# Optimization experiments

Measured on AMD Instinct MI355X. Metric: run time of the kernel, lower is better.

## Reference

```python
import jax, jax.numpy as jnp
import numpy as np

K = 20            # neighbors
C = 21            # num_classes
P = 16            # patch_size
NROWS = 14        # img_size // patch_size
H = NROWS * P     # 224
TEMP = 1.0        # temperature


def setup_inputs() -> dict:
    key = jax.random.key(0)
    k1, k2, k3 = jax.random.split(key, 3)
    test_feature = jax.random.normal(k1, (8, 196, 384), dtype=jnp.float32)
    train_features = jax.random.normal(k2, (384, 50000), dtype=jnp.float32)
    train_labels = jax.random.randint(k3, (256, 50000), 0, C, dtype=jnp.int32)
    return {"test_feature": test_feature, "train_features": train_features,
            "train_labels": train_labels}


def reference(test_feature, train_features, train_labels):
    bs = test_feature.shape[0]
    # similarity: [bs, num_patches, N_train]
    sim = jnp.einsum('bpd,dn->bpn', test_feature, train_features)
    sim_k, idx = jax.lax.top_k(sim, K)              # [bs, 196, K]
    # gather neighbor patch labels: train_labels [P^2, N] -> [bs, 196, K, P^2]
    nb = train_labels.T[idx]
    # make_grid with nrow=NROWS, padding=0: assemble patches into [bs, K, H, H]
    nb = nb.reshape(bs, NROWS, NROWS, K, P, P)
    nb = nb.transpose(0, 3, 1, 4, 2, 5).reshape(bs, K, H, H)
    nb = nb.transpose(0, 2, 3, 1)                   # [bs, H, H, K]
    # weighted majority vote: nearest-upsample similarities 14x14 -> 224x224
    w = sim_k.reshape(bs, NROWS, NROWS, K)
    w = jnp.repeat(jnp.repeat(w, P, axis=1), P, axis=2)   # [bs, H, H, K]
    w = jax.nn.softmax(w / TEMP, axis=-1)
    # one-hot vote expressed as scatter-add over classes (same math, no
    # [bs,H,H,K,C] materialization)
    rows = jnp.arange(bs * H * H)
    vote = jnp.zeros((bs * H * H, C), dtype=w.dtype)
    vote = vote.at[rows[:, None], nb.reshape(bs * H * H, K)].add(
        w.reshape(bs * H * H, K))
    vote = vote.reshape(bs, H, H, C)
    pred = jnp.argmax(vote, axis=-1)                # [bs, H, H] int
    return pred
```

## Files before the change

### kernel.cpp

```cpp
#include <hip/hip_runtime.h>
#include <float.h>

#define N_TRAIN 50000
#define NPAD    50176
#define NBLK    392
#define MPAD    1792
#define DDIM    384
#define M_ROWS  1568
#define KNN     20
#define K2      24
#define SELMAX  64
#define NCLS    21
#define CAPBUF  768
#define CBMAX   256

typedef __attribute__((ext_vector_type(8))) short bf16x8;
typedef __attribute__((ext_vector_type(4))) float f32x4;

static __device__ __forceinline__ unsigned short f2bf(float f) {
  unsigned int u = __float_as_uint(f);
  unsigned int r = (u + 0x7fffu + ((u >> 16) & 1u)) >> 16;
  return (unsigned short)r;
}
static __device__ __forceinline__ unsigned int flip32(unsigned int u) {
  return (u & 0x80000000u) ? ~u : (u | 0x80000000u);
}

__global__ __launch_bounds__(256) void transpose_labels(const int* __restrict__ labels,
                                                        unsigned char* __restrict__ labT) {
  __shared__ int tile[64][65];
  const int t  = threadIdx.x;
  const int c0 = blockIdx.x * 64;
  const int r0 = blockIdx.y * 64;
#pragma unroll
  for (int i = 0; i < 16; ++i) {
    int idx = i * 256 + t;
    int r = idx >> 6, c = idx & 63;
    int cc = c0 + c;
    tile[r][c] = (cc < N_TRAIN) ? labels[(size_t)(r0 + r) * N_TRAIN + cc] : 0;
  }
  __syncthreads();
#pragma unroll
  for (int i = 0; i < 16; ++i) {
    int idx = i * 256 + t;
    int c = idx >> 6, r = idx & 63;
    int cc = c0 + c;
    if (cc < N_TRAIN) labT[(size_t)cc * 256 + r0 + r] = (unsigned char)tile[r][c];
  }
}

__global__ __launch_bounds__(256) void conv_Apack(const float* __restrict__ test,
                                                  unsigned short* __restrict__ Apack) {
  int o = blockIdx.x * 256 + threadIdx.x;
  if (o >= (MPAD / 16) * 12 * 512) return;
  int j = o & 7;
  int l = (o >> 3) & 63;
  int kcmt = o >> 9;
  int kc = kcmt % 12, mt = kcmt / 12;
  int row = mt * 16 + (l & 15);
  int k = kc * 32 + (l >> 4) * 8 + j;
  Apack[o] = (row < M_ROWS) ? f2bf(test[(size_t)row * DDIM + k]) : (unsigned short)0;
}

__global__ __launch_bounds__(256) void trans_train_fused(const float* __restrict__ train,
                                                         unsigned short* __restrict__ Bpack,
                                                         float* __restrict__ trainT) {
  __shared__ float tile[64][65];
  const int t  = threadIdx.x;
  const int c0 = blockIdx.x * 64;
  const int r0 = blockIdx.y * 64;
#pragma unroll
  for (int i = 0; i < 16; ++i) {
    int idx = i * 256 + t;
    int r = idx >> 6, c = idx & 63;
    int cc = c0 + c;
    tile[r][c] = (cc < N_TRAIN) ? train[(size_t)(r0 + r) * N_TRAIN + cc] : 0.f;
  }
  __syncthreads();
#pragma unroll
  for (int it = 0; it < 2; ++it) {
    int u = it * 256 + t;
    int c = u & 63, koctL = u >> 6;
    int col = c0 + c;
    int koct = (r0 >> 3) + koctL;
    int kc = koct >> 2, l4 = koct & 3;
    int nt = col >> 4, l15 = col & 15;
    size_t base = ((size_t)(nt * 12 + kc) * 64 + l4 * 16 + l15) * 8;
    ushort4 h0, h1;
    h0.x = f2bf(tile[koctL * 8 + 0][c]); h0.y = f2bf(tile[koctL * 8 + 1][c]);
    h0.z = f2bf(tile[koctL * 8 + 2][c]); h0.w = f2bf(tile[koctL * 8 + 3][c]);
    h1.x = f2bf(tile[koctL * 8 + 4][c]); h1.y = f2bf(tile[koctL * 8 + 5][c]);
    h1.z = f2bf(tile[koctL * 8 + 6][c]); h1.w = f2bf(tile[koctL * 8 + 7][c]);
    *(ushort4*)&Bpack[base]     = h0;
    *(ushort4*)&Bpack[base + 4] = h1;
  }
#pragma unroll
  for (int i = 0; i < 16; ++i) {
    int idx = i * 256 + t;
    int c = idx >> 6, r = idx & 63;
    int cc = c0 + c;
    if (cc < N_TRAIN) trainT[(size_t)cc * DDIM + r0 + r] = tile[r][c];
  }
}

__global__ __launch_bounds__(256, 2) void mfma_gemm(const unsigned short* __restrict__ Apack,
                                                    const unsigned short* __restrict__ Bpack,
                                                    unsigned short* __restrict__ keybuf,
                                                    unsigned short* __restrict__ blkmax) {
  __shared__ unsigned short ct[128 * 256];
  const int t = threadIdx.x;

  const int flat = blockIdx.x;
  const int wg = (flat & 7) * 343 + (flat >> 3);
  const int mblk = wg % 14, nblk = wg / 14;
  const int m0 = mblk * 128, n0 = nblk * 256;

  const int wc = t >> 6, lane = t & 63;
  const int l15 = lane & 15, l4 = lane >> 4;

  const unsigned short* Ab = Apack + (size_t)(mblk * 8) * 12 * 512;
  const unsigned short* Bb = Bpack + (size_t)(nblk * 16 + wc * 4) * 12 * 512;

  f32x4 acc[8][4];
  const f32x4 zero = {0.f, 0.f, 0.f, 0.f};
#pragma unroll
  for (int f = 0; f < 8; ++f)
#pragma unroll
    for (int n = 0; n < 4; ++n) acc[f][n] = zero;

  for (int kc = 0; kc < 12; ++kc) {
    bf16x8 a[8], b[4];
#pragma unroll
    for (int f = 0; f < 8; ++f)
      a[f] = *(const bf16x8*)&Ab[((size_t)(f * 12 + kc) * 64 + lane) * 8];
#pragma unroll
    for (int n = 0; n < 4; ++n)
      b[n] = *(const bf16x8*)&Bb[((size_t)(n * 12 + kc) * 64 + lane) * 8];
#pragma unroll
    for (int f = 0; f < 8; ++f)
#pragma unroll
      for (int n = 0; n < 4; ++n)
        acc[f][n] = __builtin_amdgcn_mfma_f32_16x16x32_bf16(a[f], b[n], acc[f][n], 0, 0, 0);
  }

#pragma unroll
  for (int f = 0; f < 8; ++f) {
    const int row0 = f * 16 + l4 * 4;
#pragma unroll
    for (int n = 0; n < 4; ++n) {
      const int col = wc * 64 + n * 16 + l15;
      const int cl = col >> 3, ce = col & 7;
#pragma unroll
      for (int r = 0; r < 4; ++r) {
        const int rr = row0 + r;
        unsigned int k16 = flip32(__float_as_uint(acc[f][n][r])) >> 16;
        ct[rr * 256 + ((cl ^ (rr & 31)) << 3) + ce] = (unsigned short)k16;
      }
    }
  }
  __syncthreads();

  const bool boundary = (n0 + 256 > N_TRAIN);
#pragma unroll
  for (int i = 0; i < 16; ++i) {
    int idx = i * 256 + t;
    int row = idx >> 5;
    int cL  = idx & 31;
    uint4 v = *(uint4*)&ct[row * 256 + ((cL ^ (row & 31)) << 3)];
    int c8 = cL * 8;
    if (boundary) {
      int nv = N_TRAIN - (n0 + c8);
      v.x &= ((0 < nv) ? 0x0000FFFFu : 0u) | ((1 < nv) ? 0xFFFF0000u : 0u);
      v.y &= ((2 < nv) ? 0x0000FFFFu : 0u) | ((3 < nv) ? 0xFFFF0000u : 0u);
      v.z &= ((4 < nv) ? 0x0000FFFFu : 0u) | ((5 < nv) ? 0xFFFF0000u : 0u);
      v.w &= ((6 < nv) ? 0x0000FFFFu : 0u) | ((7 < nv) ? 0xFFFF0000u : 0u);
    }
    unsigned int mx = v.x & 0xFFFFu;
    mx = max(mx, v.x >> 16); mx = max(mx, v.y & 0xFFFFu); mx = max(mx, v.y >> 16);
    mx = max(mx, v.z & 0xFFFFu); mx = max(mx, v.z >> 16);
    mx = max(mx, v.w & 0xFFFFu); mx = max(mx, v.w >> 16);
    mx = max(mx, (unsigned int)__shfl_xor((int)mx, 1));
    mx = max(mx, (unsigned int)__shfl_xor((int)mx, 2));
    mx = max(mx, (unsigned int)__shfl_xor((int)mx, 4));
    mx = max(mx, (unsigned int)__shfl_xor((int)mx, 8));
    const int grow = m0 + row;
    if (grow < M_ROWS) {
      if ((lane & 15) == 0) {
        int half = (lane >> 4) & 1;
        blkmax[(size_t)grow * NBLK + nblk * 2 + half] = (unsigned short)mx;
      }
      *(uint4*)&keybuf[(size_t)grow * NPAD + n0 + c8] = v;
    }
  }
}

__global__ __launch_bounds__(256) void tail_fused(const unsigned short* __restrict__ keybuf,
                                                  const unsigned short* __restrict__ blkmax,
                                                  const float* __restrict__ test,
                                                  const float* __restrict__ trainT,
                                                  const unsigned char* __restrict__ labT,
                                                  int* __restrict__ out) {
  const int t = threadIdx.x, m = blockIdx.x;
  __shared__ unsigned short bm[NBLK];
  __shared__ int clist[CBMAX];
  __shared__ int ccnt;
  __shared__ unsigned int smax[256];
  __shared__ unsigned int sbuf[CAPBUF];
  __shared__ short srk[CAPBUF];
  __shared__ unsigned int scnt, sTauA, sTau;
  __shared__ int sC2;
  __shared__ int selC[SELMAX];
  __shared__ double rvs[SELMAX];
  __shared__ double sv2[SELMAX];
  __shared__ int    si2[SELMAX];
  __shared__ double earr[KNN];
  __shared__ double wv[KNN];
  __shared__ int    wi[KNN];

  if (t == 0) { ccnt = 0; scnt = 0u; sC2 = 0; }
  for (int i = t; i < NBLK; i += 256) bm[i] = blkmax[(size_t)m * NBLK + i];
  __syncthreads();

  for (int i = t; i < NBLK; i += 256) {
    unsigned short v = bm[i];
    int cgt = 0;
    for (int j = 0; j < NBLK; ++j) cgt += (bm[j] > v) ? 1 : 0;
    if (cgt < K2) { int p = atomicAdd(&ccnt, 1); if (p < CBMAX) clist[p] = i; }
  }
  __syncthreads();
  const int CB = min(ccnt, CBMAX);
  const int TOT = CB * 128;

  unsigned int tmx = 0u;
  for (int i = t; i < TOT; i += 256) {
    int col = clist[i >> 7] * 128 + (i & 127);
    unsigned int k = keybuf[(size_t)m * NPAD + col];
    if (k > tmx) tmx = k;
  }
  smax[t] = (tmx << 8) | (unsigned int)(255 - t);
  __syncthreads();
  {
    unsigned int myc = smax[t];
    int rnk = 0;
    for (int j = 0; j < 256; ++j) rnk += (smax[j] > myc) ? 1 : 0;
    if (rnk == K2 - 1) sTauA = myc >> 8;
  }
  __syncthreads();
  const unsigned int tauB = sTauA;

  for (int i = t; i < TOT; i += 256) {
    int col = clist[i >> 7] * 128 + (i & 127);
    unsigned int k = keybuf[(size_t)m * NPAD + col];
    if (k >= tauB) {
      unsigned int p = atomicAdd(&scnt, 1u);
      if (p < CAPBUF) sbuf[p] = (k << 16) | (unsigned int)(0xFFFF - col);
    }
  }
  __syncthreads();
  const int C = (int)min(scnt, (unsigned int)CAPBUF);

  for (int s = t; s < C; s += 256) {
    unsigned int e = sbuf[s];
    int rk = 0;
    for (int j = 0; j < C; ++j) rk += (sbuf[j] > e) ? 1 : 0;
    srk[s] = (short)rk;
    if (rk == K2 - 1) sTau = e >> 16;
  }
  __syncthreads();
  const unsigned int tau = sTau;
  for (int s = t; s < C; s += 256) {
    unsigned int e = sbuf[s];
    int rk = (int)srk[s];
    if ((e >> 16) >= tau && rk < SELMAX) {
      selC[rk] = 0xFFFF - (int)(e & 0xFFFFu);
      atomicMax(&sC2, rk + 1);
    }
  }
  __syncthreads();
  const int C2 = sC2 < SELMAX ? sC2 : SELMAX;

  const int wid = t >> 6, lane = t & 63;
  float tr[DDIM / 64];
#pragma unroll
  for (int dd = 0; dd < DDIM / 64; ++dd)
    tr[dd] = test[(size_t)m * DDIM + dd * 64 + lane];
#pragma unroll 1
  for (int c = wid; c < C2; c += 4) {
    const float* Tc = trainT + (size_t)selC[c] * DDIM;
    double s = 0.0;
#pragma unroll
    for (int dd = 0; dd < DDIM / 64; ++dd)
      s += (double)tr[dd] * (double)Tc[dd * 64 + lane];
#pragma unroll
    for (int off = 32; off > 0; off >>= 1) s += __shfl_xor(s, off);
    if (lane == 0) rvs[c] = s;
  }
  __syncthreads();

  if (t < C2) {
    double v = rvs[t]; int id = selC[t];
    int r = 0;
    for (int n = 0; n < C2; ++n)
      r += (rvs[n] > v || (rvs[n] == v && selC[n] < id)) ? 1 : 0;
    sv2[r] = v; si2[r] = id;
  }
  __syncthreads();

  if (t < KNN) earr[t] = exp(sv2[t] - sv2[0]);
  __syncthreads();
  if (t < KNN) {
    double ssum = 0.0;
    for (int k = 0; k < KNN; ++k) ssum += earr[k];
    wv[t] = earr[t] / ssum;
    wi[t] = si2[t];
  }
  __syncthreads();

  unsigned int packed[5];
#pragma unroll
  for (int q = 0; q < 5; ++q) {
    unsigned int p = 0;
#pragma unroll
    for (int j = 0; j < 4; ++j)
      p |= (unsigned int)labT[(size_t)wi[q * 4 + j] * 256 + t] << (8 * j);
    packed[q] = p;
  }
  double best = -1.0; int bc = 0;
#pragma unroll 1
  for (int c = 0; c < NCLS; ++c) {
    double s = 0.0;
#pragma unroll
    for (int k = 0; k < KNN; ++k) {
      unsigned int lab = (packed[k >> 2] >> ((k & 3) * 8)) & 255u;
      s += (lab == (unsigned int)c) ? wv[k] : 0.0;
    }
    if (s > best) { best = s; bc = c; }
  }
  const int b = m / 196, p = m % 196;
  const int py = p / 14, px = p % 14;
  const int i = t >> 4, j = t & 15;
  out[((size_t)b * 224 + py * 16 + i) * 224 + px * 16 + j] = bc;
}

extern "C" void kernel_launch(void* const* d_in, const int* in_sizes, int n_in,
                              void* d_out, int out_size, void* d_ws, size_t ws_size,
                              hipStream_t stream) {
  const float* test  = (const float*)d_in[0];
  const float* train = (const float*)d_in[1];
  const int* labels  = (const int*)d_in[2];
  int* out = (int*)d_out;
  char* ws = (char*)d_ws;

  unsigned char*  labT    = (unsigned char*)ws;
  unsigned short* Apack   = (unsigned short*)(ws + 12800000);
  unsigned short* Bpack   = (unsigned short*)(ws + 14176256);
  unsigned short* keybuf  = (unsigned short*)(ws + 52711424);
  float*          trainT  = (float*)(ws + 210063360);
  unsigned short* blkmax  = (unsigned short*)(ws + 286863360);

  transpose_labels<<<dim3(782, 4), 256, 0, stream>>>(labels, labT);
  conv_Apack<<<dim3(2688), 256, 0, stream>>>(test, Apack);
  trans_train_fused<<<dim3(784, 6), 256, 0, stream>>>(train, Bpack, trainT);
  mfma_gemm<<<dim3(2744), 256, 0, stream>>>(Apack, Bpack, keybuf, blkmax);
  tail_fused<<<dim3(M_ROWS), 256, 0, stream>>>(keybuf, blkmax, test, trainT, labT, out);
}
```

Baseline: 257.9 us.

## Fuse per-block top-4 selection into GEMM epilogue, drop full key buffer

The GEMM epilogue now computes a per-row top-4 candidate list for each 256-column block using register sorting networks and wave shuffles. It writes only these 4 entries per block instead of the full 16-bit similarity matrix and block maxima. The GEMM tile shrinks to 64 rows, with a different XCD block mapping and higher occupancy. The tail kernel selects candidates from the compact list and recomputes full column blocks with scalar dot products when a block's 4th entry reaches the threshold. This removes the large keybuf write and read traffic, at the cost of extra epilogue compute and occasional scalar recomputation in the tail.

```diff
diff --git a/kernel.cpp b/kernel.cpp
--- a/kernel.cpp
+++ b/kernel.cpp
@@ -3,8 +3,8 @@
 
 #define N_TRAIN 50000
 #define NPAD    50176
-#define NBLK    392
-#define MPAD    1792
+#define NBLKG   196
+#define MPAD    1600
 #define DDIM    384
 #define M_ROWS  1568
 #define KNN     20
@@ -12,7 +12,7 @@
 #define SELMAX  64
 #define NCLS    21
 #define CAPBUF  768
-#define CBMAX   256
+#define NENT    784
 
 typedef __attribute__((ext_vector_type(8))) short bf16x8;
 typedef __attribute__((ext_vector_type(4))) float f32x4;
@@ -22,9 +22,14 @@
   unsigned int r = (u + 0x7fffu + ((u >> 16) & 1u)) >> 16;
   return (unsigned short)r;
 }
+static __device__ __forceinline__ float bf2f(unsigned short h) {
+  return __uint_as_float(((unsigned int)h) << 16);
+}
 static __device__ __forceinline__ unsigned int flip32(unsigned int u) {
   return (u & 0x80000000u) ? ~u : (u | 0x80000000u);
 }
+
+#define CSW(x, y) { unsigned int _hi = max(x, y); unsigned int _lo = min(x, y); x = _hi; y = _lo; }
 
 __global__ __launch_bounds__(256) void transpose_labels(const int* __restrict__ labels,
                                                         unsigned char* __restrict__ labT) {
@@ -103,113 +108,117 @@
   }
 }
 
-__global__ __launch_bounds__(256, 2) void mfma_gemm(const unsigned short* __restrict__ Apack,
+__global__ __launch_bounds__(256, 3) void mfma_gemm(const unsigned short* __restrict__ Apack,
                                                     const unsigned short* __restrict__ Bpack,
-                                                    unsigned short* __restrict__ keybuf,
-                                                    unsigned short* __restrict__ blkmax) {
-  __shared__ unsigned short ct[128 * 256];
+                                                    unsigned int* __restrict__ toplist) {
+  __shared__ unsigned int ldsT[64 * 16];
   const int t = threadIdx.x;
 
   const int flat = blockIdx.x;
-  const int wg = (flat & 7) * 343 + (flat >> 3);
-  const int mblk = wg % 14, nblk = wg / 14;
-  const int m0 = mblk * 128, n0 = nblk * 256;
+  const int xcd = flat & 7, jj = flat >> 3;
+  const int wg = (xcd < 4 ? xcd * 613 : 2452 + (xcd - 4) * 612) + jj;
+  const int mblk = wg % 25, nblk = wg / 25;
+  const int m0 = mblk * 64, n0 = nblk * 256;
 
   const int wc = t >> 6, lane = t & 63;
   const int l15 = lane & 15, l4 = lane >> 4;
 
-  const unsigned short* Ab = Apack + (size_t)(mblk * 8) * 12 * 512;
+  const unsigned short* Ab = Apack + (size_t)(mblk * 4) * 12 * 512;
   const unsigned short* Bb = Bpack + (size_t)(nblk * 16 + wc * 4) * 12 * 512;
 
-  f32x4 acc[8][4];
+  f32x4 acc[4][4];
   const f32x4 zero = {0.f, 0.f, 0.f, 0.f};
 #pragma unroll
-  for (int f = 0; f < 8; ++f)
+  for (int f = 0; f < 4; ++f)
 #pragma unroll
     for (int n = 0; n < 4; ++n) acc[f][n] = zero;
 
   for (int kc = 0; kc < 12; ++kc) {
-    bf16x8 a[8], b[4];
-#pragma unroll
-    for (int f = 0; f < 8; ++f)
+    bf16x8 a[4], b[4];
+#pragma unroll
+    for (int f = 0; f < 4; ++f)
       a[f] = *(const bf16x8*)&Ab[((size_t)(f * 12 + kc) * 64 + lane) * 8];
 #pragma unroll
     for (int n = 0; n < 4; ++n)
       b[n] = *(const bf16x8*)&Bb[((size_t)(n * 12 + kc) * 64 + lane) * 8];
 #pragma unroll
-    for (int f = 0; f < 8; ++f)
+    for (int f = 0; f < 4; ++f)
 #pragma unroll
       for (int n = 0; n < 4; ++n)
         acc[f][n] = __builtin_amdgcn_mfma_f32_16x16x32_bf16(a[f], b[n], acc[f][n], 0, 0, 0);
   }
 
 #pragma unroll
-  for (int f = 0; f < 8; ++f) {
-    const int row0 = f * 16 + l4 * 4;
-#pragma unroll
-    for (int n = 0; n < 4; ++n) {
-      const int col = wc * 64 + n * 16 + l15;
-      const int cl = col >> 3, ce = col & 7;
-#pragma unroll
-      for (int r = 0; r < 4; ++r) {
-        const int rr = row0 + r;
+  for (int f = 0; f < 4; ++f) {
+#pragma unroll
+    for (int r = 0; r < 4; ++r) {
+      const int row = f * 16 + l4 * 4 + r;
+      unsigned int e[4];
+#pragma unroll
+      for (int n = 0; n < 4; ++n) {
+        int col = n0 + wc * 64 + n * 16 + l15;
         unsigned int k16 = flip32(__float_as_uint(acc[f][n][r])) >> 16;
-        ct[rr * 256 + ((cl ^ (rr & 31)) << 3) + ce] = (unsigned short)k16;
-      }
-    }
-  }
-  __syncthreads();
-
-  const bool boundary = (n0 + 256 > N_TRAIN);
-#pragma unroll
-  for (int i = 0; i < 16; ++i) {
-    int idx = i * 256 + t;
-    int row = idx >> 5;
-    int cL  = idx & 31;
-    uint4 v = *(uint4*)&ct[row * 256 + ((cL ^ (row & 31)) << 3)];
-    int c8 = cL * 8;
-    if (boundary) {
-      int nv = N_TRAIN - (n0 + c8);
-      v.x &= ((0 < nv) ? 0x0000FFFFu : 0u) | ((1 < nv) ? 0xFFFF0000u : 0u);
-      v.y &= ((2 < nv) ? 0x0000FFFFu : 0u) | ((3 < nv) ? 0xFFFF0000u : 0u);
-      v.z &= ((4 < nv) ? 0x0000FFFFu : 0u) | ((5 < nv) ? 0xFFFF0000u : 0u);
-      v.w &= ((6 < nv) ? 0x0000FFFFu : 0u) | ((7 < nv) ? 0xFFFF0000u : 0u);
-    }
-    unsigned int mx = v.x & 0xFFFFu;
-    mx = max(mx, v.x >> 16); mx = max(mx, v.y & 0xFFFFu); mx = max(mx, v.y >> 16);
-    mx = max(mx, v.z & 0xFFFFu); mx = max(mx, v.z >> 16);
-    mx = max(mx, v.w & 0xFFFFu); mx = max(mx, v.w >> 16);
-    mx = max(mx, (unsigned int)__shfl_xor((int)mx, 1));
-    mx = max(mx, (unsigned int)__shfl_xor((int)mx, 2));
-    mx = max(mx, (unsigned int)__shfl_xor((int)mx, 4));
-    mx = max(mx, (unsigned int)__shfl_xor((int)mx, 8));
-    const int grow = m0 + row;
+        e[n] = (col < N_TRAIN) ? ((k16 << 16) | (0xFFFFu - (unsigned int)col)) : 0u;
+      }
+      CSW(e[0], e[1]); CSW(e[2], e[3]); CSW(e[0], e[2]); CSW(e[1], e[3]); CSW(e[1], e[2]);
+#pragma unroll
+      for (int st = 1; st <= 8; st <<= 1) {
+        unsigned int p0 = (unsigned int)__shfl_xor((int)e[0], st);
+        unsigned int p1 = (unsigned int)__shfl_xor((int)e[1], st);
+        unsigned int p2 = (unsigned int)__shfl_xor((int)e[2], st);
+        unsigned int p3 = (unsigned int)__shfl_xor((int)e[3], st);
+        unsigned int t0 = max(e[0], p3), t1 = max(e[1], p2);
+        unsigned int t2 = max(e[2], p1), t3 = max(e[3], p0);
+        CSW(t0, t2); CSW(t1, t3); CSW(t0, t1); CSW(t2, t3);
+        e[0] = t0; e[1] = t1; e[2] = t2; e[3] = t3;
+      }
+      if (l15 == 0) {
+        uint4 v; v.x = e[0]; v.y = e[1]; v.z = e[2]; v.w = e[3];
+        *(uint4*)&ldsT[row * 16 + wc * 4] = v;
+      }
+    }
+  }
+  __syncthreads();
+
+  if (t < 64) {
+    const int grow = m0 + t;
     if (grow < M_ROWS) {
-      if ((lane & 15) == 0) {
-        int half = (lane >> 4) & 1;
-        blkmax[(size_t)grow * NBLK + nblk * 2 + half] = (unsigned short)mx;
-      }
-      *(uint4*)&keybuf[(size_t)grow * NPAD + n0 + c8] = v;
-    }
-  }
-}
-
-__global__ __launch_bounds__(256) void tail_fused(const unsigned short* __restrict__ keybuf,
-                                                  const unsigned short* __restrict__ blkmax,
+      unsigned int v[16];
+#pragma unroll
+      for (int q = 0; q < 4; ++q)
+        *(uint4*)&v[q * 4] = *(uint4*)&ldsT[t * 16 + q * 4];
+      unsigned int o0 = 0, o1 = 0, o2 = 0, o3 = 0;
+#pragma unroll
+      for (int j = 0; j < 16; ++j) {
+        int rk = 0;
+#pragma unroll
+        for (int k = 0; k < 16; ++k) rk += (v[k] > v[j]) ? 1 : 0;
+        if (rk == 0) o0 = v[j];
+        else if (rk == 1) o1 = v[j];
+        else if (rk == 2) o2 = v[j];
+        else if (rk == 3) o3 = v[j];
+      }
+      uint4 w; w.x = o0; w.y = o1; w.z = o2; w.w = o3;
+      *(uint4*)&toplist[(size_t)grow * NENT + nblk * 4] = w;
+    }
+  }
+}
+
+__global__ __launch_bounds__(256) void tail_fused(const unsigned int* __restrict__ toplist,
                                                   const float* __restrict__ test,
                                                   const float* __restrict__ trainT,
                                                   const unsigned char* __restrict__ labT,
                                                   int* __restrict__ out) {
   const int t = threadIdx.x, m = blockIdx.x;
-  __shared__ unsigned short bm[NBLK];
-  __shared__ int clist[CBMAX];
-  __shared__ int ccnt;
+  __shared__ unsigned int ent[NENT];
   __shared__ unsigned int smax[256];
   __shared__ unsigned int sbuf[CAPBUF];
-  __shared__ short srk[CAPBUF];
-  __shared__ unsigned int scnt, sTauA, sTau;
-  __shared__ int sC2;
-  __shared__ int selC[SELMAX];
+  __shared__ unsigned int scnt, sTauA, sE24, ccnt2;
+  __shared__ unsigned char flg[NBLKG];
+  __shared__ short flist[NBLKG];
+  __shared__ int fcnt, sC2;
+  __shared__ unsigned int cbuf[128];
+  __shared__ int    selC[SELMAX];
   __shared__ double rvs[SELMAX];
   __shared__ double sv2[SELMAX];
   __shared__ int    si2[SELMAX];
@@ -217,61 +226,80 @@
   __shared__ double wv[KNN];
   __shared__ int    wi[KNN];
 
-  if (t == 0) { ccnt = 0; scnt = 0u; sC2 = 0; }
-  for (int i = t; i < NBLK; i += 256) bm[i] = blkmax[(size_t)m * NBLK + i];
-  __syncthreads();
-
-  for (int i = t; i < NBLK; i += 256) {
-    unsigned short v = bm[i];
-    int cgt = 0;
-    for (int j = 0; j < NBLK; ++j) cgt += (bm[j] > v) ? 1 : 0;
-    if (cgt < K2) { int p = atomicAdd(&ccnt, 1); if (p < CBMAX) clist[p] = i; }
-  }
-  __syncthreads();
-  const int CB = min(ccnt, CBMAX);
-  const int TOT = CB * 128;
-
-  unsigned int tmx = 0u;
-  for (int i = t; i < TOT; i += 256) {
-    int col = clist[i >> 7] * 128 + (i & 127);
-    unsigned int k = keybuf[(size_t)m * NPAD + col];
-    if (k > tmx) tmx = k;
-  }
-  smax[t] = (tmx << 8) | (unsigned int)(255 - t);
+  if (t == 0) { scnt = 0u; fcnt = 0; ccnt2 = 0u; sC2 = 0; }
+  for (int i = t; i < NENT; i += 256) ent[i] = toplist[(size_t)m * NENT + i];
+  __syncthreads();
+
+  unsigned int mx = 0u;
+  for (int i = t; i < NENT; i += 256) mx = max(mx, ent[i]);
+  smax[t] = mx;
   __syncthreads();
   {
-    unsigned int myc = smax[t];
     int rnk = 0;
-    for (int j = 0; j < 256; ++j) rnk += (smax[j] > myc) ? 1 : 0;
-    if (rnk == K2 - 1) sTauA = myc >> 8;
-  }
-  __syncthreads();
-  const unsigned int tauB = sTauA;
-
-  for (int i = t; i < TOT; i += 256) {
-    int col = clist[i >> 7] * 128 + (i & 127);
-    unsigned int k = keybuf[(size_t)m * NPAD + col];
-    if (k >= tauB) {
-      unsigned int p = atomicAdd(&scnt, 1u);
-      if (p < CAPBUF) sbuf[p] = (k << 16) | (unsigned int)(0xFFFF - col);
-    }
+    for (int j = 0; j < 256; ++j)
+      rnk += (smax[j] > mx || (smax[j] == mx && j < t)) ? 1 : 0;
+    if (rnk == K2 - 1) sTauA = mx;
+  }
+  __syncthreads();
+  const unsigned int tauA = sTauA;
+
+  for (int i = t; i < NENT; i += 256) {
+    unsigned int e = ent[i];
+    if (e >= tauA) { unsigned int p = atomicAdd(&scnt, 1u); if (p < CAPBUF) sbuf[p] = e; }
   }
   __syncthreads();
   const int C = (int)min(scnt, (unsigned int)CAPBUF);
-
   for (int s = t; s < C; s += 256) {
     unsigned int e = sbuf[s];
     int rk = 0;
     for (int j = 0; j < C; ++j) rk += (sbuf[j] > e) ? 1 : 0;
-    srk[s] = (short)rk;
-    if (rk == K2 - 1) sTau = e >> 16;
-  }
-  __syncthreads();
-  const unsigned int tau = sTau;
-  for (int s = t; s < C; s += 256) {
-    unsigned int e = sbuf[s];
-    int rk = (int)srk[s];
-    if ((e >> 16) >= tau && rk < SELMAX) {
+    if (rk == K2 - 1) sE24 = e;
+  }
+  __syncthreads();
+  const unsigned int k24 = sE24 >> 16;
+
+  if (t < NBLKG) {
+    bool fl = (ent[t * 4 + 3] >> 16) >= k24;
+    flg[t] = fl ? 1 : 0;
+    if (fl) { int p = atomicAdd(&fcnt, 1); flist[p] = (short)t; }
+  }
+  __syncthreads();
+
+  for (int i = t; i < NENT; i += 256) {
+    unsigned int e = ent[i];
+    if ((e >> 16) >= k24) {
+      int col = 0xFFFF - (int)(e & 0xFFFFu);
+      if (!flg[col >> 8]) { unsigned int p = atomicAdd(&ccnt2, 1u); if (p < 128) cbuf[p] = e; }
+    }
+  }
+  __syncthreads();
+
+  const int FC = fcnt;
+  for (int q = 0; q < FC; ++q) {
+    const int fb = flist[q];
+    const int col = fb * 256 + t;
+    if (col < N_TRAIN) {
+      const float* Tc = trainT + (size_t)col * DDIM;
+      const float* Tr = test + (size_t)m * DDIM;
+      float s0 = 0.f;
+      for (int k = 0; k < DDIM; ++k)
+        s0 = fmaf(bf2f(f2bf(Tr[k])), bf2f(f2bf(Tc[k])), s0);
+      unsigned int key = flip32(__float_as_uint(s0)) >> 16;
+      if (key + 1u >= k24) {
+        unsigned int e = (key << 16) | (0xFFFFu - (unsigned int)col);
+        unsigned int p = atomicAdd(&ccnt2, 1u);
+        if (p < 128) cbuf[p] = e;
+      }
+    }
+  }
+  __syncthreads();
+  const int CC = (int)min(ccnt2, 128u);
+
+  for (int s = t; s < CC; s += 256) {
+    unsigned int e = cbuf[s];
+    int rk = 0;
+    for (int j = 0; j < CC; ++j) rk += (cbuf[j] > e) ? 1 : 0;
+    if (rk < SELMAX) {
       selC[rk] = 0xFFFF - (int)(e & 0xFFFFu);
       atomicMax(&sC2, rk + 1);
     }
@@ -353,14 +381,13 @@
 
   unsigned char*  labT    = (unsigned char*)ws;
   unsigned short* Apack   = (unsigned short*)(ws + 12800000);
-  unsigned short* Bpack   = (unsigned short*)(ws + 14176256);
-  unsigned short* keybuf  = (unsigned short*)(ws + 52711424);
-  float*          trainT  = (float*)(ws + 210063360);
-  unsigned short* blkmax  = (unsigned short*)(ws + 286863360);
+  unsigned short* Bpack   = (unsigned short*)(ws + 14028800);
+  float*          trainT  = (float*)(ws + 52563968);
+  unsigned int*   toplist = (unsigned int*)(ws + 129363968);
 
   transpose_labels<<<dim3(782, 4), 256, 0, stream>>>(labels, labT);
-  conv_Apack<<<dim3(2688), 256, 0, stream>>>(test, Apack);
+  conv_Apack<<<dim3((MPAD / 16) * 12 * 512 / 256), 256, 0, stream>>>(test, Apack);
   trans_train_fused<<<dim3(784, 6), 256, 0, stream>>>(train, Bpack, trainT);
-  mfma_gemm<<<dim3(2744), 256, 0, stream>>>(Apack, Bpack, keybuf, blkmax);
-  tail_fused<<<dim3(M_ROWS), 256, 0, stream>>>(keybuf, blkmax, test, trainT, labT, out);
-}
+  mfma_gemm<<<dim3(25 * NBLKG), 256, 0, stream>>>(Apack, Bpack, toplist);
+  tail_fused<<<dim3(M_ROWS), 256, 0, stream>>>(toplist, test, trainT, labT, out);
+}
```

After: 238.1 us. 1.08x faster.
